# Kernel tuning notes

Hardware: AMD Instinct MI355X
Metric: run time of the kernel (lower is better)

## Reference

```python
import jax, jax.numpy as jnp
import numpy as np

B, H, W = 16, 512, 512
N_BINS = 511          # round(mean(shape)) - 1 for (512, 512)
MAX_R = 1.0           # (1 + min(shape)/max(shape)) / 2 for square image


def _bin_ids():
    # Precompute per-pixel radial shell index (replaces the list of boolean shell masks).
    frame = max(H, W)
    xx, yy = np.mgrid[:H, :W]
    ellipse = ((xx - H / 2) * 2 / frame) ** 2 + ((yy - W / 2) * 2 / frame) ** 2
    r2 = np.linspace(0.0, MAX_R, N_BINS + 1)[1:] ** 2
    # shell k = { r2[k-1] <= ellipse < r2[k] }; pixels with ellipse >= r2[-1] map to
    # overflow bin N_BINS and are dropped, exactly matching the xor'd ellipse masks.
    return jnp.asarray(np.searchsorted(r2, ellipse.ravel(), side='right').astype(np.int32))


BIN_IDS = _bin_ids()  # [H*W] int32 in [0, N_BINS]


def setup_inputs() -> dict:
    key = jax.random.key(0)
    k1, k2 = jax.random.split(key)
    return {
        "z_": jax.random.normal(k1, (B, H, W, 2), dtype=jnp.float32),
        "t_": jax.random.normal(k2, (B, H, W, 2), dtype=jnp.float32),
    }


def _shell_sums(x):
    # x: [B, H*W] -> per-shell sums [B, N_BINS+1] in a single fused segment-sum pass.
    return jax.vmap(lambda v: jax.ops.segment_sum(v, BIN_IDS, num_segments=N_BINS + 1))(x)


def reference(z_, t_):
    tc = t_[..., 0] + 1j * t_[..., 1]          # [B,H,W] complex target
    zc = z_[..., 0] + 1j * z_[..., 1]
    Ft = jnp.fft.fft2(tc, axes=(-2, -1))
    Fe = jnp.fft.fft2(zc - tc, axes=(-2, -1))
    norm_coeff = Ft.real ** 2 + Ft.imag ** 2   # |FFT(target)|^2, [B,H,W]
    errors = Fe.real ** 2 + Fe.imag ** 2       # |FFT(z - target)|^2
    es = _shell_sums(errors.reshape(B, -1))[:, :N_BINS]      # drop overflow bin
    ns = _shell_sums(norm_coeff.reshape(B, -1))[:, :N_BINS]
    nre = es / jnp.maximum(ns, 1e-8)           # per-batch, per-shell normed error
    # per_shell_loss = per-batch sum over shells; loss = mean over batch
    return jnp.mean(jnp.sum(nre, axis=1))
```

## Files before the change

### kernel.cpp

```cpp
#include <hip/hip_runtime.h>

#define HH 512
#define WW 512
#define NBATCH 16
#define NBINS 512

#define PI_F 3.14159265358979323846f

#define SW(r) ((r) ^ (((r) >> 4) & 0xF))
#define TSW(c, hh) (((c) << 3) + ((hh) ^ (((c) >> 1) & 7)))

#define DPP_SHR(x, n) __builtin_amdgcn_update_dpp(0, (x), 0x110 + (n), 0xF, 0xF, true)
#define DPP_SHL1(x)   __builtin_amdgcn_update_dpp(0, (x), 0x101,       0xF, 0xF, true)

__device__ __forceinline__ float2 cadd(float2 a, float2 b){ return make_float2(a.x+b.x, a.y+b.y); }
__device__ __forceinline__ float2 csub(float2 a, float2 b){ return make_float2(a.x-b.x, a.y-b.y); }
__device__ __forceinline__ float2 cmul(float2 a, float2 b){
    return make_float2(a.x*b.x - a.y*b.y, a.x*b.y + a.y*b.x);
}

__device__ __forceinline__ void dft8(const float2* a, float2* y) {
    const float s2 = 0.70710678118654752440f;
    float2 t02a = cadd(a[0], a[4]), t02s = csub(a[0], a[4]);
    float2 t13a = cadd(a[2], a[6]), t13s = csub(a[2], a[6]);
    float2 E0 = cadd(t02a, t13a);
    float2 E2 = csub(t02a, t13a);
    float2 E1 = make_float2(t02s.x + t13s.y, t02s.y - t13s.x);
    float2 E3 = make_float2(t02s.x - t13s.y, t02s.y + t13s.x);
    float2 u02a = cadd(a[1], a[5]), u02s = csub(a[1], a[5]);
    float2 u13a = cadd(a[3], a[7]), u13s = csub(a[3], a[7]);
    float2 O0 = cadd(u02a, u13a);
    float2 O2 = csub(u02a, u13a);
    float2 O1 = make_float2(u02s.x + u13s.y, u02s.y - u13s.x);
    float2 O3 = make_float2(u02s.x - u13s.y, u02s.y + u13s.x);
    float2 wO1 = make_float2(s2 * (O1.x + O1.y), s2 * (O1.y - O1.x));
    float2 wO2 = make_float2(O2.y, -O2.x);
    float2 wO3 = make_float2(s2 * (O3.y - O3.x), -s2 * (O3.x + O3.y));
    y[0] = cadd(E0, O0);  y[4] = csub(E0, O0);
    y[1] = cadd(E1, wO1); y[5] = csub(E1, wO1);
    y[2] = cadd(E2, wO2); y[6] = csub(E2, wO2);
    y[3] = cadd(E3, wO3); y[7] = csub(E3, wO3);
}

__device__ __forceinline__ void twiddle8(float base, float2* w) {
    float s1, c1, s4, c4;
    __sincosf(base, &s1, &c1);
    __sincosf(4.0f * base, &s4, &c4);
    w[0] = make_float2(1.0f, 0.0f);
    w[1] = make_float2(c1, s1);
    w[2] = cmul(w[1], w[1]);
    w[3] = cmul(w[2], w[1]);
    w[4] = make_float2(c4, s4);
    w[5] = cmul(w[4], w[1]);
    w[6] = cmul(w[4], w[2]);
    w[7] = cmul(w[4], w[3]);
}

__device__ __forceinline__ void fft512_stage0_store(float2* rb, int lane, const float2* a) {
    float2 y[8]; dft8(a, y);
    float2 w[8]; twiddle8(-PI_F * (float)lane * (1.0f / 256.0f), w);
#pragma unroll
    for (int r = 0; r < 8; ++r) rb[SW(8 * lane + r)] = cmul(y[r], w[r]);
}

__device__ __forceinline__ void fft512_stage1(float2* rb, int lane) {
    float2 a[8];
#pragma unroll
    for (int u = 0; u < 8; ++u) a[u] = rb[SW(lane + 64 * u)];
    float2 y[8]; dft8(a, y);
    float2 w[8]; twiddle8(-PI_F * (float)(lane >> 3) * (1.0f / 32.0f), w);
    const int qb = (lane & 7) + ((lane >> 3) << 6);
#pragma unroll
    for (int r = 0; r < 8; ++r) rb[SW(qb + 8 * r)] = cmul(y[r], w[r]);
}

__device__ __forceinline__ void fft512_stage2(const float2* rb, int lane, float2* y) {
    float2 a[8];
#pragma unroll
    for (int u = 0; u < 8; ++u) a[u] = rb[SW(lane + 64 * u)];
    dft8(a, y);
}

__global__ __launch_bounds__(512, 4)
void row_fft_kernel(const float2* __restrict__ z, const float2* __restrict__ t,
                    float2* __restrict__ fieldsT, int b0) {
    __shared__ float2 buf[8 * 512];
    const int tid  = threadIdx.x;
    const int lane = tid & 63;
    const int g    = tid >> 6;
    const int bid  = blockIdx.x;
    const int hg   = bid & 63;
    const int lb   = bid >> 6;
    const int b    = b0 + lb;
    const int h    = (hg << 3) | g;
    const size_t rowOff = ((size_t)(b * HH + h)) * WW;

    const float2* tr = t + rowOff;
    const float2* zr = z + rowOff;
    float2 tv[8], zv[8];
#pragma unroll
    for (int u = 0; u < 8; ++u) tv[u] = tr[lane + 64 * u];
#pragma unroll
    for (int u = 0; u < 8; ++u) zv[u] = zr[lane + 64 * u];

    float2* rb = buf + (g << 9);
#pragma unroll
    for (int f = 0; f < 2; ++f) {
        float2 a[8];
        if (f == 0) {
#pragma unroll
            for (int u = 0; u < 8; ++u) a[u] = tv[u];
        } else {
#pragma unroll
            for (int u = 0; u < 8; ++u) a[u] = make_float2(zv[u].x - tv[u].x,
                                                           zv[u].y - tv[u].y);
        }
        fft512_stage0_store(rb, lane, a);
        __builtin_amdgcn_wave_barrier();
        fft512_stage1(rb, lane);
        __builtin_amdgcn_wave_barrier();
        float2 y[8];
        fft512_stage2(rb, lane, y);

        __syncthreads();
#pragma unroll
        for (int r = 0; r < 8; ++r) {
            int c = lane + (r << 6);
            buf[TSW(c, g)] = y[r];
        }
        __syncthreads();
        float2* outF = fieldsT + ((size_t)(lb * 2 + f) << 18);
#pragma unroll
        for (int k = 0; k < 8; ++k) {
            int e  = tid + (k << 9);
            int c  = e >> 3;
            int hh = e & 7;
            outF[((size_t)c << 9) + (hg << 3) + hh] = buf[TSW(c, hh)];
        }
        __syncthreads();
    }
}

__global__ __launch_bounds__(512, 4)
void col_fft_bin_kernel(const float2* __restrict__ fieldsT,
                        float* __restrict__ partials, int b0) {
    __shared__ float2 buf[8 * 512];
    const int tid  = threadIdx.x;
    const int lane = tid & 63;
    const int g    = tid >> 6;
    const int bid  = blockIdx.x;
    const int cg   = bid & 63;
    const int lb   = bid >> 6;
    const int b    = b0 + lb;
    const int c    = (cg << 3) | g;

    const float2* colA = fieldsT + (((size_t)(lb * 2 + 0) << 9) + c) * 512;
    const float2* colB = fieldsT + (((size_t)(lb * 2 + 1) << 9) + c) * 512;

    float2* rb = buf + (g << 9);

    float2 a[8];
#pragma unroll
    for (int u = 0; u < 8; ++u) a[u] = colA[lane + (u << 6)];
    fft512_stage0_store(rb, lane, a);
    float2 bB[8];
#pragma unroll
    for (int u = 0; u < 8; ++u) bB[u] = colB[lane + (u << 6)];
    __builtin_amdgcn_wave_barrier();
    fft512_stage1(rb, lane);
    __builtin_amdgcn_wave_barrier();
    float2 y[8];
    fft512_stage2(rb, lane, y);
    float pA[8];
#pragma unroll
    for (int r = 0; r < 8; ++r) pA[r] = y[r].x * y[r].x + y[r].y * y[r].y;
    __builtin_amdgcn_wave_barrier();
    __asm__ volatile("" ::: "memory");

    fft512_stage0_store(rb, lane, bB);
    __builtin_amdgcn_wave_barrier();
    fft512_stage1(rb, lane);
    __builtin_amdgcn_wave_barrier();
    fft512_stage2(rb, lane, y);
    __builtin_amdgcn_wave_barrier();
    __asm__ volatile("" ::: "memory");

#pragma unroll
    for (int j = 0; j < 8; ++j) rb[lane + (j << 6)] = make_float2(0.0f, 0.0f);
    __builtin_amdgcn_wave_barrier();
    __asm__ volatile("" ::: "memory");

    float* histA = (float*)rb;
    float* histB = histA + 512;
    const int dc = c - 256;
    const unsigned fc2i = (unsigned)(dc * dc);
    const int l15 = lane & 15;
#pragma unroll
    for (int r = 0; r < 8; ++r) {
        int k  = lane + (r << 6);
        int dk = k - 256;
        unsigned m = (unsigned)(dk * dk) + fc2i;
        int bin = (int)(sqrtf((float)m) * (511.0f / 256.0f));
        unsigned long long rhs = 261121ull * (unsigned long long)m;
        unsigned bp1 = (unsigned)(bin + 1);
        if (((unsigned long long)(bp1 * bp1) << 16) <= rhs) ++bin;
        else if (((unsigned long long)((unsigned)bin * (unsigned)bin) << 16) > rhs) --bin;
        bin = (m < 65536u) ? bin : 511;

        float v = pA[r];
        float w = y[r].x * y[r].x + y[r].y * y[r].y;

        int nb; bool take;
        nb = DPP_SHR(bin, 1); take = (l15 >= 1 && nb == bin);
        v += take ? __int_as_float(DPP_SHR(__float_as_int(v), 1)) : 0.0f;
        w += take ? __int_as_float(DPP_SHR(__float_as_int(w), 1)) : 0.0f;
        nb = DPP_SHR(bin, 2); take = (l15 >= 2 && nb == bin);
        v += take ? __int_as_float(DPP_SHR(__float_as_int(v), 2)) : 0.0f;
        w += take ? __int_as_float(DPP_SHR(__float_as_int(w), 2)) : 0.0f;
        nb = DPP_SHR(bin, 4); take = (l15 >= 4 && nb == bin);
        v += take ? __int_as_float(DPP_SHR(__float_as_int(v), 4)) : 0.0f;
        w += take ? __int_as_float(DPP_SHR(__float_as_int(w), 4)) : 0.0f;
        nb = DPP_SHR(bin, 8); take = (l15 >= 8 && nb == bin);
        v += take ? __int_as_float(DPP_SHR(__float_as_int(v), 8)) : 0.0f;
        w += take ? __int_as_float(DPP_SHR(__float_as_int(w), 8)) : 0.0f;

        int nxt = DPP_SHL1(bin);
        if (l15 == 15 || nxt != bin) {
            atomicAdd(&histA[bin], v);
            atomicAdd(&histB[bin], w);
        }
    }
    __syncthreads();

    const float* bufF = (const float*)buf;
    float sA = 0.0f, sB = 0.0f;
#pragma unroll
    for (int gg = 0; gg < 8; ++gg) {
        sA += bufF[(gg << 10) + tid];
        sB += bufF[(gg << 10) + 512 + tid];
    }
    partials[(((size_t)cg << 5) + (size_t)b) * NBINS + tid] = sA;
    partials[(((size_t)cg << 5) + (size_t)(NBATCH + b)) * NBINS + tid] = sB;
}

__global__ __launch_bounds__(512)
void reduce_bins_kernel(const float* __restrict__ partials, float* __restrict__ bins) {
    __shared__ float red[512];
    const int tid = threadIdx.x;
    const int fl  = blockIdx.x >> 2;
    const int q   = blockIdx.x & 3;
    const int bin = (q << 7) + (tid & 127);
    const int ch  = tid >> 7;
    float s = 0.0f;
#pragma unroll
    for (int j = 0; j < 16; ++j) {
        int cg = (ch << 4) + j;
        s += partials[((size_t)(cg << 5) + fl) * NBINS + bin];
    }
    red[tid] = s;
    __syncthreads();
    if (tid < 128) {
        bins[(size_t)fl * NBINS + bin] =
            red[tid] + red[tid + 128] + red[tid + 256] + red[tid + 384];
    }
}

__global__ __launch_bounds__(512)
void loss_kernel(const float* __restrict__ bins, float* __restrict__ outp) {
    __shared__ float red[512];
    const int tid = threadIdx.x;
    float acc = 0.0f;
    if (tid < 511) {
#pragma unroll 4
        for (int b = 0; b < NBATCH; ++b) {
            float ns = bins[((size_t)b) * NBINS + tid];
            float es = bins[((size_t)(NBATCH + b)) * NBINS + tid];
            acc += es / fmaxf(ns, 1e-8f);
        }
    }
    red[tid] = acc;
    __syncthreads();
    for (int s = 256; s > 0; s >>= 1) {
        if (tid < s) red[tid] += red[tid + s];
        __syncthreads();
    }
    if (tid == 0) outp[0] = red[0] * (1.0f / NBATCH);
}

extern "C" void kernel_launch(void* const* d_in, const int* in_sizes, int n_in,
                              void* d_out, int out_size, void* d_ws, size_t ws_size,
                              hipStream_t stream) {
    const float2* z = (const float2*)d_in[0];
    const float2* t = (const float2*)d_in[1];
    float* outp = (float*)d_out;

    const size_t partialsBytes = 64ull * 2 * NBATCH * NBINS * sizeof(float);
    const size_t binsBytes     = (size_t)2 * NBATCH * NBINS * sizeof(float);
    const size_t fixedBytes    = partialsBytes + binsBytes;
    const size_t fpb = (size_t)2 * HH * WW * sizeof(float2);

    int CB = 16;
    while (CB > 1 && fixedBytes + (size_t)CB * fpb > ws_size) CB >>= 1;

    float*  partials = (float*)d_ws;
    float*  bins     = (float*)((char*)d_ws + partialsBytes);
    float2* fieldsT  = (float2*)((char*)d_ws + fixedBytes);

    for (int b0 = 0; b0 < NBATCH; b0 += CB) {
        row_fft_kernel<<<CB * 64, 512, 0, stream>>>(z, t, fieldsT, b0);
        col_fft_bin_kernel<<<CB * 64, 512, 0, stream>>>(fieldsT, partials, b0);
    }
    reduce_bins_kernel<<<128, 512, 0, stream>>>(partials, bins);
    loss_kernel<<<1, 512, 0, stream>>>(bins, outp);
}
```

Measured before the change: 160.8 us.

## Interleave both column FFTs per wave and shrink column blocks to four waves

The column FFT kernel now has each wave run the A and B column transforms together, one stage at a time, in separate LDS regions. Before, the two transforms ran one after the other, and the interleaving is meant to expose more independent work per wave and hide LDS latency. Blocks shrink from 512 to 256 threads (4 columns each), which doubles the block count and the partial-histogram rows. The bin reduction kernel becomes a simple 32-block loop over 128 partials. The cost is higher register pressure from holding both transforms live, and twice as much partials traffic.

Measured after the change: 165.0 us. 1.03x slower.

```diff
diff --git a/kernel.cpp b/kernel.cpp
--- a/kernel.cpp
+++ b/kernel.cpp
@@ -4,6 +4,7 @@
 #define WW 512
 #define NBATCH 16
 #define NBINS 512
+#define NCQ 128
 
 #define PI_F 3.14159265358979323846f
 
@@ -81,6 +82,51 @@
     dft8(a, y);
 }
 
+__device__ __forceinline__ void dual_stage0(float2* rbA, float2* rbB, int lane,
+                                            const float2* aA, const float2* aB) {
+    float2 yA[8]; dft8(aA, yA);
+    float2 yB[8]; dft8(aB, yB);
+    float2 w[8]; twiddle8(-PI_F * (float)lane * (1.0f / 256.0f), w);
+#pragma unroll
+    for (int r = 0; r < 8; ++r) {
+        rbA[SW(8 * lane + r)] = cmul(yA[r], w[r]);
+        rbB[SW(8 * lane + r)] = cmul(yB[r], w[r]);
+    }
+}
+
+__device__ __forceinline__ void dual_stage1(float2* rbA, float2* rbB, int lane) {
+    float2 aA[8], aB[8];
+#pragma unroll
+    for (int u = 0; u < 8; ++u) aA[u] = rbA[SW(lane + 64 * u)];
+#pragma unroll
+    for (int u = 0; u < 8; ++u) aB[u] = rbB[SW(lane + 64 * u)];
+    float2 yA[8]; dft8(aA, yA);
+    float2 yB[8]; dft8(aB, yB);
+    float2 w[8]; twiddle8(-PI_F * (float)(lane >> 3) * (1.0f / 32.0f), w);
+    const int qb = (lane & 7) + ((lane >> 3) << 6);
+#pragma unroll
+    for (int r = 0; r < 8; ++r) {
+        rbA[SW(qb + 8 * r)] = cmul(yA[r], w[r]);
+        rbB[SW(qb + 8 * r)] = cmul(yB[r], w[r]);
+    }
+}
+
+__device__ __forceinline__ void dual_stage2(const float2* rbA, const float2* rbB,
+                                            int lane, float* pA, float* pB) {
+    float2 aA[8], aB[8];
+#pragma unroll
+    for (int u = 0; u < 8; ++u) aA[u] = rbA[SW(lane + 64 * u)];
+#pragma unroll
+    for (int u = 0; u < 8; ++u) aB[u] = rbB[SW(lane + 64 * u)];
+    float2 yA[8]; dft8(aA, yA);
+    float2 yB[8]; dft8(aB, yB);
+#pragma unroll
+    for (int r = 0; r < 8; ++r) {
+        pA[r] = yA[r].x * yA[r].x + yA[r].y * yA[r].y;
+        pB[r] = yB[r].x * yB[r].x + yB[r].y * yB[r].y;
+    }
+}
+
 __global__ __launch_bounds__(512, 4)
 void row_fft_kernel(const float2* __restrict__ z, const float2* __restrict__ t,
                     float2* __restrict__ fieldsT, int b0) {
@@ -141,57 +187,49 @@
     }
 }
 
-__global__ __launch_bounds__(512, 4)
+__global__ __launch_bounds__(256, 4)
 void col_fft_bin_kernel(const float2* __restrict__ fieldsT,
                         float* __restrict__ partials, int b0) {
-    __shared__ float2 buf[8 * 512];
+    __shared__ float2 buf[4 * 2 * 512];
     const int tid  = threadIdx.x;
     const int lane = tid & 63;
     const int g    = tid >> 6;
     const int bid  = blockIdx.x;
-    const int cg   = bid & 63;
-    const int lb   = bid >> 6;
+    const int cq   = bid & (NCQ - 1);
+    const int lb   = bid >> 7;
     const int b    = b0 + lb;
-    const int c    = (cg << 3) | g;
+    const int c    = (cq << 2) | g;
 
     const float2* colA = fieldsT + (((size_t)(lb * 2 + 0) << 9) + c) * 512;
     const float2* colB = fieldsT + (((size_t)(lb * 2 + 1) << 9) + c) * 512;
-
-    float2* rb = buf + (g << 9);
-
-    float2 a[8];
-#pragma unroll
-    for (int u = 0; u < 8; ++u) a[u] = colA[lane + (u << 6)];
-    fft512_stage0_store(rb, lane, a);
-    float2 bB[8];
-#pragma unroll
-    for (int u = 0; u < 8; ++u) bB[u] = colB[lane + (u << 6)];
+    float2 aA[8], aB[8];
+#pragma unroll
+    for (int u = 0; u < 8; ++u) aA[u] = colA[lane + (u << 6)];
+#pragma unroll
+    for (int u = 0; u < 8; ++u) aB[u] = colB[lane + (u << 6)];
+
+    float2* rbA = buf + (g << 10);
+    float2* rbB = rbA + 512;
+
+    dual_stage0(rbA, rbB, lane, aA, aB);
     __builtin_amdgcn_wave_barrier();
-    fft512_stage1(rb, lane);
+    dual_stage1(rbA, rbB, lane);
     __builtin_amdgcn_wave_barrier();
-    float2 y[8];
-    fft512_stage2(rb, lane, y);
-    float pA[8];
-#pragma unroll
-    for (int r = 0; r < 8; ++r) pA[r] = y[r].x * y[r].x + y[r].y * y[r].y;
+    float pA[8], pB[8];
+    dual_stage2(rbA, rbB, lane, pA, pB);
     __builtin_amdgcn_wave_barrier();
     __asm__ volatile("" ::: "memory");
 
-    fft512_stage0_store(rb, lane, bB);
-    __builtin_amdgcn_wave_barrier();
-    fft512_stage1(rb, lane);
-    __builtin_amdgcn_wave_barrier();
-    fft512_stage2(rb, lane, y);
+#pragma unroll
+    for (int j = 0; j < 4; ++j) {
+        rbA[lane + (j << 6)] = make_float2(0.0f, 0.0f);
+        rbB[lane + (j << 6)] = make_float2(0.0f, 0.0f);
+    }
     __builtin_amdgcn_wave_barrier();
     __asm__ volatile("" ::: "memory");
 
-#pragma unroll
-    for (int j = 0; j < 8; ++j) rb[lane + (j << 6)] = make_float2(0.0f, 0.0f);
-    __builtin_amdgcn_wave_barrier();
-    __asm__ volatile("" ::: "memory");
-
-    float* histA = (float*)rb;
-    float* histB = histA + 512;
+    float* histA = (float*)rbA;
+    float* histB = (float*)rbB;
     const int dc = c - 256;
     const unsigned fc2i = (unsigned)(dc * dc);
     const int l15 = lane & 15;
@@ -208,7 +246,7 @@
         bin = (m < 65536u) ? bin : 511;
 
         float v = pA[r];
-        float w = y[r].x * y[r].x + y[r].y * y[r].y;
+        float w = pB[r];
 
         int nb; bool take;
         nb = DPP_SHR(bin, 1); take = (l15 >= 1 && nb == bin);
@@ -233,36 +271,30 @@
     __syncthreads();
 
     const float* bufF = (const float*)buf;
-    float sA = 0.0f, sB = 0.0f;
-#pragma unroll
-    for (int gg = 0; gg < 8; ++gg) {
-        sA += bufF[(gg << 10) + tid];
-        sB += bufF[(gg << 10) + 512 + tid];
-    }
-    partials[(((size_t)cg << 5) + (size_t)b) * NBINS + tid] = sA;
-    partials[(((size_t)cg << 5) + (size_t)(NBATCH + b)) * NBINS + tid] = sB;
+    float sA0 = 0.0f, sA1 = 0.0f, sB0 = 0.0f, sB1 = 0.0f;
+#pragma unroll
+    for (int w = 0; w < 4; ++w) {
+        const int base = w << 11;
+        sA0 += bufF[base + tid];
+        sA1 += bufF[base + 256 + tid];
+        sB0 += bufF[base + 1024 + tid];
+        sB1 += bufF[base + 1024 + 256 + tid];
+    }
+    float* dA = partials + ((size_t)(cq << 5) + (size_t)b) * NBINS;
+    float* dB = partials + ((size_t)(cq << 5) + (size_t)(NBATCH + b)) * NBINS;
+    dA[tid] = sA0; dA[tid + 256] = sA1;
+    dB[tid] = sB0; dB[tid + 256] = sB1;
 }
 
 __global__ __launch_bounds__(512)
 void reduce_bins_kernel(const float* __restrict__ partials, float* __restrict__ bins) {
-    __shared__ float red[512];
     const int tid = threadIdx.x;
-    const int fl  = blockIdx.x >> 2;
-    const int q   = blockIdx.x & 3;
-    const int bin = (q << 7) + (tid & 127);
-    const int ch  = tid >> 7;
+    const int fl  = blockIdx.x;
     float s = 0.0f;
-#pragma unroll
-    for (int j = 0; j < 16; ++j) {
-        int cg = (ch << 4) + j;
-        s += partials[((size_t)(cg << 5) + fl) * NBINS + bin];
-    }
-    red[tid] = s;
-    __syncthreads();
-    if (tid < 128) {
-        bins[(size_t)fl * NBINS + bin] =
-            red[tid] + red[tid + 128] + red[tid + 256] + red[tid + 384];
-    }
+#pragma unroll 8
+    for (int cq = 0; cq < NCQ; ++cq)
+        s += partials[((size_t)(cq << 5) + fl) * NBINS + tid];
+    bins[(size_t)fl * NBINS + tid] = s;
 }
 
 __global__ __launch_bounds__(512)
@@ -294,7 +326,7 @@
     const float2* t = (const float2*)d_in[1];
     float* outp = (float*)d_out;
 
-    const size_t partialsBytes = 64ull * 2 * NBATCH * NBINS * sizeof(float);
+    const size_t partialsBytes = (size_t)NCQ * 2 * NBATCH * NBINS * sizeof(float);
     const size_t binsBytes     = (size_t)2 * NBATCH * NBINS * sizeof(float);
     const size_t fixedBytes    = partialsBytes + binsBytes;
     const size_t fpb = (size_t)2 * HH * WW * sizeof(float2);
@@ -308,8 +340,8 @@
 
     for (int b0 = 0; b0 < NBATCH; b0 += CB) {
         row_fft_kernel<<<CB * 64, 512, 0, stream>>>(z, t, fieldsT, b0);
-        col_fft_bin_kernel<<<CB * 64, 512, 0, stream>>>(fieldsT, partials, b0);
-    }
-    reduce_bins_kernel<<<128, 512, 0, stream>>>(partials, bins);
+        col_fft_bin_kernel<<<CB * NCQ, 256, 0, stream>>>(fieldsT, partials, b0);
+    }
+    reduce_bins_kernel<<<32, 512, 0, stream>>>(partials, bins);
     loss_kernel<<<1, 512, 0, stream>>>(bins, outp);
 }
```

## Split column FFT and binning into separate kernels with interleaved column layout

Applied to the files above, without the earlier changes.

Splits the fused column-FFT-plus-binning kernel in two. The first kernel computes one field's column FFT per block (twice as many blocks) and writes power spectra to a new workspace buffer; the second loads both power arrays and does the histogram binning. The row-FFT output layout is changed to interleave column pairs, and the batch chunk size drops from 16 to 4 with more kernel launches. This is meant to raise parallelism and register headroom in the FFT kernel, at the cost of an extra global write and read of the power arrays and more launches.

After: 202.8 us. +26.1%, slower.

```diff
diff --git a/kernel.cpp b/kernel.cpp
--- a/kernel.cpp
+++ b/kernel.cpp
@@ -4,6 +4,7 @@
 #define WW 512
 #define NBATCH 16
 #define NBINS 512
+#define NCG 64
 
 #define PI_F 3.14159265358979323846f
 
@@ -135,56 +136,68 @@
             int e  = tid + (k << 9);
             int c  = e >> 3;
             int hh = e & 7;
-            outF[((size_t)c << 9) + (hg << 3) + hh] = buf[TSW(c, hh)];
+            int hr = (hg << 3) | hh;
+            outF[((size_t)(c >> 1) << 10) + (hr << 1) + (c & 1)] = buf[TSW(c, hh)];
         }
         __syncthreads();
     }
 }
 
 __global__ __launch_bounds__(512, 4)
-void col_fft_bin_kernel(const float2* __restrict__ fieldsT,
-                        float* __restrict__ partials, int b0) {
+void colfft_kernel(const float2* __restrict__ fieldsT,
+                   float* __restrict__ pow_) {
     __shared__ float2 buf[8 * 512];
     const int tid  = threadIdx.x;
     const int lane = tid & 63;
     const int g    = tid >> 6;
     const int bid  = blockIdx.x;
-    const int cg   = bid & 63;
-    const int lb   = bid >> 6;
-    const int b    = b0 + lb;
+    const int cg   = bid & (NCG - 1);
+    const int f    = (bid >> 6) & 1;
+    const int lb   = bid >> 7;
     const int c    = (cg << 3) | g;
 
-    const float2* colA = fieldsT + (((size_t)(lb * 2 + 0) << 9) + c) * 512;
-    const float2* colB = fieldsT + (((size_t)(lb * 2 + 1) << 9) + c) * 512;
+    const float2* colT = fieldsT + ((size_t)(lb * 2 + f) << 18)
+                                 + ((size_t)(c >> 1) << 10) + (c & 1);
+    float2 a[8];
+#pragma unroll
+    for (int u = 0; u < 8; ++u) a[u] = colT[(lane + (u << 6)) << 1];
 
     float2* rb = buf + (g << 9);
-
-    float2 a[8];
-#pragma unroll
-    for (int u = 0; u < 8; ++u) a[u] = colA[lane + (u << 6)];
     fft512_stage0_store(rb, lane, a);
-    float2 bB[8];
-#pragma unroll
-    for (int u = 0; u < 8; ++u) bB[u] = colB[lane + (u << 6)];
     __builtin_amdgcn_wave_barrier();
     fft512_stage1(rb, lane);
     __builtin_amdgcn_wave_barrier();
     float2 y[8];
     fft512_stage2(rb, lane, y);
-    float pA[8];
-#pragma unroll
-    for (int r = 0; r < 8; ++r) pA[r] = y[r].x * y[r].x + y[r].y * y[r].y;
-    __builtin_amdgcn_wave_barrier();
-    __asm__ volatile("" ::: "memory");
-
-    fft512_stage0_store(rb, lane, bB);
-    __builtin_amdgcn_wave_barrier();
-    fft512_stage1(rb, lane);
-    __builtin_amdgcn_wave_barrier();
-    fft512_stage2(rb, lane, y);
-    __builtin_amdgcn_wave_barrier();
-    __asm__ volatile("" ::: "memory");
-
+
+    float* outp = pow_ + ((size_t)(lb * 2 + f) << 18) + ((size_t)c << 9);
+#pragma unroll
+    for (int r = 0; r < 8; ++r)
+        outp[lane + (r << 6)] = y[r].x * y[r].x + y[r].y * y[r].y;
+}
+
+__global__ __launch_bounds__(512, 4)
+void bin_kernel(const float* __restrict__ pow_,
+                float* __restrict__ partials, int b0) {
+    __shared__ float2 buf[8 * 512];
+    const int tid  = threadIdx.x;
+    const int lane = tid & 63;
+    const int g    = tid >> 6;
+    const int bid  = blockIdx.x;
+    const int cg   = bid & (NCG - 1);
+    const int lb   = bid >> 6;
+    const int b    = b0 + lb;
+    const int c    = (cg << 3) | g;
+
+    const float* pN = pow_ + ((size_t)(lb * 2 + 0) << 18) + ((size_t)c << 9);
+    const float* pE = pow_ + ((size_t)(lb * 2 + 1) << 18) + ((size_t)c << 9);
+    float pA[8], pB[8];
+#pragma unroll
+    for (int u = 0; u < 8; ++u) pA[u] = pN[lane + (u << 6)];
+#pragma unroll
+    for (int u = 0; u < 8; ++u) pB[u] = pE[lane + (u << 6)];
+
+    float2* rb = buf + (g << 9);
 #pragma unroll
     for (int j = 0; j < 8; ++j) rb[lane + (j << 6)] = make_float2(0.0f, 0.0f);
     __builtin_amdgcn_wave_barrier();
@@ -208,7 +221,7 @@
         bin = (m < 65536u) ? bin : 511;
 
         float v = pA[r];
-        float w = y[r].x * y[r].x + y[r].y * y[r].y;
+        float w = pB[r];
 
         int nb; bool take;
         nb = DPP_SHR(bin, 1); take = (l15 >= 1 && nb == bin);
@@ -294,21 +307,24 @@
     const float2* t = (const float2*)d_in[1];
     float* outp = (float*)d_out;
 
-    const size_t partialsBytes = 64ull * 2 * NBATCH * NBINS * sizeof(float);
+    const size_t partialsBytes = (size_t)NCG * 2 * NBATCH * NBINS * sizeof(float);
     const size_t binsBytes     = (size_t)2 * NBATCH * NBINS * sizeof(float);
     const size_t fixedBytes    = partialsBytes + binsBytes;
     const size_t fpb = (size_t)2 * HH * WW * sizeof(float2);
-
-    int CB = 16;
-    while (CB > 1 && fixedBytes + (size_t)CB * fpb > ws_size) CB >>= 1;
+    const size_t ppb = (size_t)2 * HH * WW * sizeof(float);
+
+    int CB = 4;
+    while (CB > 1 && fixedBytes + (size_t)CB * (fpb + ppb) > ws_size) CB >>= 1;
 
     float*  partials = (float*)d_ws;
     float*  bins     = (float*)((char*)d_ws + partialsBytes);
     float2* fieldsT  = (float2*)((char*)d_ws + fixedBytes);
+    float*  pow_     = (float*)((char*)d_ws + fixedBytes + (size_t)CB * fpb);
 
     for (int b0 = 0; b0 < NBATCH; b0 += CB) {
         row_fft_kernel<<<CB * 64, 512, 0, stream>>>(z, t, fieldsT, b0);
-        col_fft_bin_kernel<<<CB * 64, 512, 0, stream>>>(fieldsT, partials, b0);
+        colfft_kernel<<<CB * 2 * 64, 512, 0, stream>>>(fieldsT, pow_);
+        bin_kernel<<<CB * 64, 512, 0, stream>>>(pow_, partials, b0);
     }
     reduce_bins_kernel<<<128, 512, 0, stream>>>(partials, bins);
     loss_kernel<<<1, 512, 0, stream>>>(bins, outp);
```
